# Kernel optimization log

Hardware: AMD Instinct MI355X
Metric: run time of the kernel (lower is better)

Reference implementation:

```python
import jax, jax.numpy as jnp
import numpy as np
from jax import lax

ITERATIONS = 8
GAMMA = 0.99
TEMPERATURE = 100.0
THRESHOLD_SCALE = 2.0
MIN_SOURCE = 1e-06


def maxpool3(x):
    # 3x3 max pool, stride 1, pad 1 (pad value -inf, matching torch MaxPool2d)
    return lax.reduce_window(x, -jnp.inf, lax.max, (1, 1, 3, 3), (1, 1, 1, 1),
                             [(0, 0), (0, 0), (1, 1), (1, 1)])


def _axis_coords(n_out, n_in, dtype):
    if n_out == 1:
        return jnp.zeros((1,), dtype=dtype)
    return jnp.arange(n_out, dtype=dtype) * ((n_in - 1) / (n_out - 1))


def resize_bilinear(x, out_h, out_w):
    # bilinear resize with align_corners=True, separable along H then W
    B, C, H, W = x.shape
    dt = x.dtype
    h = _axis_coords(out_h, H, dt)
    i0 = jnp.floor(h).astype(jnp.int32)
    i1 = jnp.minimum(i0 + 1, H - 1)
    wh = (h - i0.astype(dt))[None, None, :, None]
    x = x[:, :, i0, :] * (1 - wh) + x[:, :, i1, :] * wh
    w = _axis_coords(out_w, W, dt)
    j0 = jnp.floor(w).astype(jnp.int32)
    j1 = jnp.minimum(j0 + 1, W - 1)
    ww = (w - j0.astype(dt))[None, None, None, :]
    x = x[:, :, :, j0] * (1 - ww) + x[:, :, :, j1] * ww
    return x


def activation_mask(m):
    B, C, H, W = m.shape
    flat = m.reshape(B, C, H * W)
    mean = lax.stop_gradient(jnp.mean(flat, axis=-1))
    std = lax.stop_gradient(jnp.std(flat, axis=-1, ddof=1))  # torch std is unbiased
    thr = (mean + THRESHOLD_SCALE * std)[:, :, None, None]
    return jax.nn.sigmoid(TEMPERATURE * (m - thr)) + MIN_SOURCE


def propagate_field(init_field):
    B, C, H, W = init_field.shape
    cur = init_field
    down = maxpool3(init_field) * GAMMA  # level 0, stride 1
    cur = jnp.maximum(cur, down)
    stride = 1
    h, w = H, W
    for _ in range(1, ITERATIONS):
        stride *= 2
        h, w = h // 2, w // 2  # floor(size * 0.5)
        down = resize_bilinear(down, h, w)
        down = maxpool3(down) * (GAMMA ** stride)
        up = resize_bilinear(down, H, W)
        cur = jnp.maximum(cur, up)
    return cur


def setup_inputs() -> dict:
    key = jax.random.key(0)
    k1, k2, k3 = jax.random.split(key, 3)
    B, C, H, W = 4, 128, 256, 256
    Cm = C // 8
    x = jax.random.normal(k1, (B, C, H, W), dtype=jnp.float32)
    w1 = jax.random.normal(k2, (Cm, C), dtype=jnp.float32) * 0.05
    b1 = jnp.zeros((Cm,), dtype=jnp.float32)
    w2 = jax.random.normal(k3, (C, Cm), dtype=jnp.float32) * 0.05
    b2 = jnp.zeros((C,), dtype=jnp.float32)
    return {"x": x, "w1": w1, "b1": b1, "w2": w2, "b2": b2}


def reference(x, w1, b1, w2, b2):
    x_pos = jax.nn.relu(x)
    x_neg = jax.nn.relu(-x)
    L_pos = propagate_field(x_pos * activation_mask(x_pos))
    L_neg = propagate_field(x_neg * activation_mask(x_neg))
    radiance = L_pos - L_neg
    # receptor modulator: 1x1 conv -> relu -> 1x1 conv -> sigmoid
    h = jax.nn.relu(jnp.einsum('oc,bchw->bohw', w1, radiance) + b1[None, :, None, None])
    mod = jax.nn.sigmoid(jnp.einsum('oc,bchw->bohw', w2, h) + b2[None, :, None, None])
    return x * mod
```

## Files before the change

### kernel.cpp

```cpp
#include <hip/hip_runtime.h>
#include <cmath>

constexpr int BN = 4, CN = 128, HN = 256, WN = 256;
constexpr int NPLANE = BN * CN;
constexpr int PLANE  = HN * WN;

constexpr long long OF_THR = 0;
constexpr long long OF_R1  = 1024;
constexpr long long OF_D1  = OF_R1 + 2LL * NPLANE * 128 * 128;
constexpr long long OF_D2  = OF_D1 + 2LL * NPLANE * 128 * 128;
constexpr long long OF_D3  = OF_D2 + 2LL * NPLANE * 64 * 64;
constexpr long long OF_D4  = OF_D3 + 2LL * NPLANE * 32 * 32;
constexpr long long OF_D5  = OF_D4 + 2LL * NPLANE * 16 * 16;
constexpr long long OF_D6  = OF_D5 + 2LL * NPLANE * 8 * 8;
constexpr long long OF_D7  = OF_D6 + 2LL * NPLANE * 4 * 4;

static __device__ __forceinline__ float sigm100(float a, float thr) {
    return 1.f / (1.f + __expf(-100.f * (a - thr))) + 1e-6f;
}

__global__ __launch_bounds__(256) void statsA_kernel(const float* __restrict__ x,
                                                     float* __restrict__ ws) {
    const int strip = blockIdx.x;
    const int p = blockIdx.y;
    const int tid = threadIdx.x;
    const float* xp = x + (long long)p * PLANE + strip * 4096;
    float sp = 0, spp = 0, sn = 0, snn = 0;
    for (int i = tid; i < 4096; i += 256) {
        float v = xp[i];
        float a = fmaxf(v, 0.f), b = fmaxf(-v, 0.f);
        sp += a; spp += a * a;
        sn += b; snn += b * b;
    }
    __shared__ float red[256];
    float vals[4] = {sp, spp, sn, snn};
    float* dst = ws + OF_D1 + ((long long)p * 16 + strip) * 4;
    for (int q = 0; q < 4; q++) {
        red[tid] = vals[q];
        __syncthreads();
        for (int s = 128; s > 0; s >>= 1) {
            if (tid < s) red[tid] += red[tid + s];
            __syncthreads();
        }
        if (tid == 0) dst[q] = red[0];
        __syncthreads();
    }
}

__global__ __launch_bounds__(256) void statsB_kernel(float* __restrict__ ws) {
    int p = blockIdx.x * 256 + threadIdx.x;
    if (p >= 512) return;
    double sp = 0, spp = 0, sn = 0, snn = 0;
    for (int s = 0; s < 16; s++) {
        const float* src = ws + OF_D1 + ((long long)p * 16 + s) * 4;
        sp += src[0]; spp += src[1]; sn += src[2]; snn += src[3];
    }
    double N = (double)PLANE;
    double meanP = sp / N, meanN = sn / N;
    double varP = (spp - sp * sp / N) / (N - 1.0);
    double varN = (snn - sn * sn / N) / (N - 1.0);
    varP = varP > 0 ? varP : 0;
    varN = varN > 0 ? varN : 0;
    ws[OF_THR + p]       = (float)(meanP + 2.0 * sqrt(varP));
    ws[OF_THR + 512 + p] = (float)(meanN + 2.0 * sqrt(varN));
}

__global__ __launch_bounds__(256, 3) void field_kernel(const float* __restrict__ x,
                                                       float* __restrict__ ws) {
    const int tile = blockIdx.x;
    const int p = blockIdx.y;
    const int ty = tile >> 2, tx = tile & 3;
    const int y0 = ty * 64, x0 = tx * 64;
    const int tid = threadIdx.x;

    __shared__ float cf[66 * 66];
    __shared__ float plP[64 * 64];
    __shared__ float plN[64 * 64];

    const float thrP = ws[OF_THR + p];
    const float thrN = ws[OF_THR + 512 + p];
    const float* xp = x + (long long)p * PLANE;

    for (int i = tid; i < 66 * 66; i += 256) {
        int ly = i / 66, lx = i - ly * 66;
        int gy = min(max(y0 - 1 + ly, 0), 255);
        int gx = min(max(x0 - 1 + lx, 0), 255);
        float v = xp[gy * 256 + gx];
        float thr = v > 0.f ? thrP : thrN;
        cf[i] = v * sigm100(fabsf(v), thr);
    }
    __syncthreads();

    const float g1 = 0.99f;
    for (int i = tid; i < 64 * 64; i += 256) {
        int oy = i >> 6, ox = i & 63;
        const float* r0 = cf + oy * 66 + ox;
        const float* r1r = r0 + 66;
        const float* r2 = r1r + 66;
        float cmax = fmaxf(fmaxf(r0[0], r0[1]), r0[2]);
        float cmin = fminf(fminf(r0[0], r0[1]), r0[2]);
        cmax = fmaxf(cmax, fmaxf(fmaxf(r1r[0], r1r[1]), r1r[2]));
        cmin = fminf(cmin, fminf(fminf(r1r[0], r1r[1]), r1r[2]));
        cmax = fmaxf(cmax, fmaxf(fmaxf(r2[0], r2[1]), r2[2]));
        cmin = fminf(cmin, fminf(fminf(r2[0], r2[1]), r2[2]));
        plP[i] = fmaxf(cmax, 0.f) * g1;
        plN[i] = fmaxf(-cmin, 0.f) * g1;
    }
    __syncthreads();

    const float S = (float)(255.0 / 127.0);
    for (int i = tid; i < 32 * 32; i += 256) {
        int ry = i >> 5, rx = i & 31;
        int jy = ty * 32 + ry, jx = tx * 32 + rx;
        float uy = jy * S, ux = jx * S;
        int iy0 = (int)floorf(uy), ix0 = (int)floorf(ux);
        int iy1 = min(iy0 + 1, 255), ix1 = min(ix0 + 1, 255);
        float fy = uy - iy0, fx = ux - ix0;
        int ly0 = min(max(iy0 - y0, 0), 63), ly1 = min(max(iy1 - y0, 0), 63);
        int lx0 = min(max(ix0 - x0, 0), 63), lx1 = min(max(ix1 - x0, 0), 63);
        float aP = plP[ly0 * 64 + lx0], bP = plP[ly0 * 64 + lx1];
        float cP = plP[ly1 * 64 + lx0], dP = plP[ly1 * 64 + lx1];
        float vP = (aP * (1.f - fy) + cP * fy) * (1.f - fx) + (bP * (1.f - fy) + dP * fy) * fx;
        float aN = plN[ly0 * 64 + lx0], bN = plN[ly0 * 64 + lx1];
        float cN = plN[ly1 * 64 + lx0], dN = plN[ly1 * 64 + lx1];
        float vN = (aN * (1.f - fy) + cN * fy) * (1.f - fx) + (bN * (1.f - fy) + dN * fy) * fx;
        ws[OF_R1 + (long long)p * 16384 + jy * 128 + jx] = vP;
        ws[OF_R1 + (long long)(512 + p) * 16384 + jy * 128 + jx] = vN;
    }
}

__global__ __launch_bounds__(256) void pool1_kernel(float* __restrict__ ws, float gamma2) {
    long long gid = (long long)blockIdx.x * 256 + threadIdx.x;
    int ps = (int)(gid >> 14);
    int rem = (int)(gid & 16383);
    int oy = rem >> 7, ox = rem & 127;
    const float* src = ws + OF_R1 + (long long)ps * 16384;
    float m = -INFINITY;
    for (int dy = -1; dy <= 1; dy++) {
        int yy = oy + dy;
        if (yy < 0 || yy > 127) continue;
        for (int dx = -1; dx <= 1; dx++) {
            int xx = ox + dx;
            if (xx < 0 || xx > 127) continue;
            m = fmaxf(m, src[yy * 128 + xx]);
        }
    }
    ws[OF_D1 + (long long)ps * 16384 + rem] = m * gamma2;
}

__global__ __launch_bounds__(256) void pstep_kernel(float* __restrict__ ws,
                                                    long long srcOff, long long dstOff,
                                                    int m, int n, int logn,
                                                    float scale, float gamma) {
    int gid = blockIdx.x * 256 + threadIdx.x;
    int ps = gid >> (2 * logn);
    int rem = gid & ((1 << (2 * logn)) - 1);
    int oy = rem >> logn, ox = rem & ((1 << logn) - 1);
    const float* src = ws + srcOff + (long long)ps * m * m;
    float best = -INFINITY;
    for (int dy = -1; dy <= 1; dy++) {
        int yy = oy + dy;
        if (yy < 0 || yy >= n) continue;
        float uy = yy * scale;
        int iy0 = (int)floorf(uy);
        if (iy0 > m - 1) iy0 = m - 1;
        int iy1 = min(iy0 + 1, m - 1);
        float fy = uy - iy0;
        for (int dx = -1; dx <= 1; dx++) {
            int xx = ox + dx;
            if (xx < 0 || xx >= n) continue;
            float ux = xx * scale;
            int ix0 = (int)floorf(ux);
            if (ix0 > m - 1) ix0 = m - 1;
            int ix1 = min(ix0 + 1, m - 1);
            float fx = ux - ix0;
            float a = src[iy0 * m + ix0], b = src[iy0 * m + ix1];
            float c = src[iy1 * m + ix0], d = src[iy1 * m + ix1];
            float v = (a * (1.f - fy) + c * fy) * (1.f - fx) + (b * (1.f - fy) + d * fy) * fx;
            best = fmaxf(best, v);
        }
    }
    ws[dstOff + (long long)ps * n * n + rem] = best * gamma;
}

__global__ __launch_bounds__(256, 4) void radiance_kernel(const float* __restrict__ x,
                                                          const float* __restrict__ ws,
                                                          float* __restrict__ rad) {
    const int tY = blockIdx.x;
    const int p = blockIdx.y;
    const int Y0 = tY * 16;
    const int tid = threadIdx.x;

    __shared__ float cf[18 * 258];
    __shared__ float fpb[2 * 1920];

    const float thrP = ws[OF_THR + p];
    const float thrN = ws[OF_THR + 512 + p];
    const float* xp = x + (long long)p * PLANE;

    for (int r = 0; r < 18; r++) {
        int gy = min(max(Y0 - 1 + r, 0), 255);
        float v = xp[gy * 256 + tid];
        float thr = v > 0.f ? thrP : thrN;
        float c = v * sigm100(fabsf(v), thr);
        cf[r * 258 + tid + 1] = c;
        if (tid == 0) cf[r * 258] = c;
        if (tid == 255) cf[r * 258 + 257] = c;
    }

    int oyk[8], hyk[8], basek[8];
    int acc = 0;
#pragma unroll
    for (int k = 1; k <= 7; k++) {
        int n = 256 >> k;
        float sc = (float)(n - 1) / 255.f;
        int oy = (int)floorf(Y0 * sc);
        int ey = (int)floorf((Y0 + 15) * sc) + 1;
        if (ey > n - 1) ey = n - 1;
        oyk[k] = oy; hyk[k] = ey - oy + 1; basek[k] = acc;
        acc += hyk[k] * n;
    }
    const long long OFD[8] = {0, OF_D1, OF_D2, OF_D3, OF_D4, OF_D5, OF_D6, OF_D7};
    for (int s = 0; s < 2; s++) {
#pragma unroll
        for (int k = 1; k <= 7; k++) {
            int n = 256 >> k;
            const float* src = ws + OFD[k] + (long long)(s * 512 + p) * n * n + oyk[k] * n;
            float* dst = fpb + s * 1920 + basek[k];
            int tot = hyk[k] * n;
            for (int i = tid; i < tot; i += 256) dst[i] = src[i];
        }
    }
    __syncthreads();

    int j0[8], j1[8]; float fxk[8];
#pragma unroll
    for (int k = 1; k <= 7; k++) {
        int n = 256 >> k;
        float sc = (float)(n - 1) / 255.f;
        float ux = tid * sc;
        int a = (int)ux; if (a > n - 1) a = n - 1;
        j0[k] = a; j1[k] = min(a + 1, n - 1);
        fxk[k] = ux - (float)a;
    }

    float xl0P[8], xl1P[8], xl0N[8], xl1N[8];
    int cy[8];
#pragma unroll
    for (int k = 1; k <= 7; k++) {
        int n = 256 >> k;
        int i0 = oyk[k];
        int i1 = min(i0 + 1, n - 1);
        cy[k] = i0;
        int r1o = (i1 - oyk[k]) * n;
        float aP = fpb[basek[k] + j0[k]],        bP = fpb[basek[k] + j1[k]];
        float cP = fpb[basek[k] + r1o + j0[k]],  dP = fpb[basek[k] + r1o + j1[k]];
        xl0P[k] = aP + fxk[k] * (bP - aP);
        xl1P[k] = cP + fxk[k] * (dP - cP);
        float aN = fpb[1920 + basek[k] + j0[k]],       bN = fpb[1920 + basek[k] + j1[k]];
        float cN = fpb[1920 + basek[k] + r1o + j0[k]], dN = fpb[1920 + basek[k] + r1o + j1[k]];
        xl0N[k] = aN + fxk[k] * (bN - aN);
        xl1N[k] = cN + fxk[k] * (dN - cN);
    }

    float hx0, hx1, hx2, hn0, hn1, hn2, cc1, cc2;
    {
        int b0 = 0 * 258 + tid;
        float a = cf[b0], b = cf[b0 + 1], c = cf[b0 + 2];
        hx0 = fmaxf(fmaxf(a, b), c); hn0 = fminf(fminf(a, b), c);
        int b1 = 1 * 258 + tid;
        float d = cf[b1], e = cf[b1 + 1], f = cf[b1 + 2];
        hx1 = fmaxf(fmaxf(d, e), f); hn1 = fminf(fminf(d, e), f);
        cc1 = e;
    }

    float* radp = rad + (long long)p * PLANE + (long long)Y0 * 256 + tid;

    for (int q = 0; q < 16; q++) {
        int bn = (q + 2) * 258 + tid;
        float a = cf[bn], b = cf[bn + 1], c = cf[bn + 2];
        hx2 = fmaxf(fmaxf(a, b), c); hn2 = fminf(fminf(a, b), c);
        cc2 = b;

        float poolmax = fmaxf(fmaxf(hx0, hx1), hx2);
        float poolmin = fminf(fminf(hn0, hn1), hn2);
        float mP = fmaxf(fmaxf(cc1, 0.f), 0.99f * fmaxf(poolmax, 0.f));
        float mN = fmaxf(fmaxf(-cc1, 0.f), 0.99f * fmaxf(-poolmin, 0.f));

        int row = Y0 + q;
#pragma unroll
        for (int k = 1; k <= 7; k++) {
            int n = 256 >> k;
            float sc = (float)(n - 1) / 255.f;
            float uy = row * sc;
            int i0 = (int)uy;
            if (i0 != cy[k]) {
                cy[k] = i0;
                xl0P[k] = xl1P[k]; xl0N[k] = xl1N[k];
                int i1 = min(i0 + 1, n - 1);
                int ro = (i1 - oyk[k]) * n;
                float aP = fpb[basek[k] + ro + j0[k]], bP = fpb[basek[k] + ro + j1[k]];
                xl1P[k] = aP + fxk[k] * (bP - aP);
                float aN = fpb[1920 + basek[k] + ro + j0[k]], bN = fpb[1920 + basek[k] + ro + j1[k]];
                xl1N[k] = aN + fxk[k] * (bN - aN);
            }
            float fy = uy - (float)i0;
            mP = fmaxf(mP, xl0P[k] + fy * (xl1P[k] - xl0P[k]));
            mN = fmaxf(mN, xl0N[k] + fy * (xl1N[k] - xl0N[k]));
        }
        radp[q * 256] = mP - mN;

        hx0 = hx1; hx1 = hx2;
        hn0 = hn1; hn1 = hn2;
        cc1 = cc2;
    }
}

__global__ __launch_bounds__(256) void mlp_kernel(const float* __restrict__ x,
                                                  const float* __restrict__ w1,
                                                  const float* __restrict__ b1,
                                                  const float* __restrict__ w2,
                                                  const float* __restrict__ b2,
                                                  float* io) {
    const int y = blockIdx.x;
    const int b = blockIdx.y;
    const int col = threadIdx.x;

    float h[16];
#pragma unroll
    for (int o = 0; o < 16; o++) h[o] = b1[o];
    for (int c = 0; c < 128; c++) {
        float r = io[(long long)(b * 128 + c) * PLANE + y * 256 + col];
#pragma unroll
        for (int o = 0; o < 16; o++) h[o] += w1[o * 128 + c] * r;
    }
#pragma unroll
    for (int o = 0; o < 16; o++) h[o] = fmaxf(h[o], 0.f);
    for (int c = 0; c < 128; c++) {
        float z = b2[c];
#pragma unroll
        for (int o = 0; o < 16; o++) z += w2[c * 16 + o] * h[o];
        float mod = 1.f / (1.f + __expf(-z));
        long long idx = (long long)(b * 128 + c) * PLANE + y * 256 + col;
        io[idx] = x[idx] * mod;
    }
}

extern "C" void kernel_launch(void* const* d_in, const int* in_sizes, int n_in,
                              void* d_out, int out_size, void* d_ws, size_t ws_size,
                              hipStream_t stream) {
    (void)in_sizes; (void)n_in; (void)out_size; (void)ws_size;
    const float* x  = (const float*)d_in[0];
    const float* w1 = (const float*)d_in[1];
    const float* b1 = (const float*)d_in[2];
    const float* w2 = (const float*)d_in[3];
    const float* b2 = (const float*)d_in[4];
    float* out = (float*)d_out;
    float* ws = (float*)d_ws;

    statsA_kernel<<<dim3(16, 512), 256, 0, stream>>>(x, ws);
    statsB_kernel<<<2, 256, 0, stream>>>(ws);
    field_kernel<<<dim3(16, 512), 256, 0, stream>>>(x, ws);
    pool1_kernel<<<(1024 * 16384) / 256, 256, 0, stream>>>(ws, (float)std::pow(0.99, 2.0));

    const long long dsts[8] = {0, OF_D1, OF_D2, OF_D3, OF_D4, OF_D5, OF_D6, OF_D7};
    for (int k = 2; k <= 7; k++) {
        int m = 256 >> (k - 1), n = 256 >> k;
        int logn = 8 - k;
        float scale = (float)((double)(m - 1) / (double)(n - 1));
        float gamma = (float)std::pow(0.99, (double)(1 << k));
        int total = 1024 * n * n;
        pstep_kernel<<<total / 256, 256, 0, stream>>>(ws, dsts[k - 1], dsts[k],
                                                      m, n, logn, scale, gamma);
    }
    radiance_kernel<<<dim3(16, 512), 256, 0, stream>>>(x, ws, out);
    mlp_kernel<<<dim3(256, 4), 256, 0, stream>>>(x, w1, b1, w2, b2, out);
}
```

Baseline: 880.2 us.

## Fuse pyramid levels into one LDS-resident kernel and stream level-1 rows in radiance

Replaces the pool1 launch and the six pstep launches with a single pyramid_kernel. It builds each plane's whole downsample pyramid in shared memory and writes every level to global memory. field_kernel now computes the 3x3 pool directly at the four bilinear taps instead of staging full pooled tiles in LDS, which frees shared memory and raises the occupancy hint. radiance_kernel no longer stages the large level-1 slab; it double-buffers two 128-wide rows from global memory as needed, adding barriers inside the row loop. The intent is to remove launch overhead and global round trips between pyramid levels and to raise occupancy, at the cost of 1024 fairly heavy single-plane blocks with large LDS use.

```diff
diff --git a/kernel.cpp b/kernel.cpp
--- a/kernel.cpp
+++ b/kernel.cpp
@@ -65,7 +65,19 @@
     ws[OF_THR + 512 + p] = (float)(meanN + 2.0 * sqrt(varN));
 }
 
-__global__ __launch_bounds__(256, 3) void field_kernel(const float* __restrict__ x,
+#define POOL9(LY, LX, MX, MN)                                                 \
+    {   const float* q_ = cf + (LY) * 66 + (LX);                              \
+        float t0 = q_[0],   t1 = q_[1],   t2 = q_[2];                         \
+        float u0 = q_[66],  u1 = q_[67],  u2 = q_[68];                        \
+        float w0 = q_[132], w1 = q_[133], w2 = q_[134];                       \
+        MX = fmaxf(fmaxf(fmaxf(t0, t1), t2),                                  \
+             fmaxf(fmaxf(fmaxf(u0, u1), u2),                                  \
+                   fmaxf(fmaxf(w0, w1), w2)));                                \
+        MN = fminf(fminf(fminf(t0, t1), t2),                                  \
+             fminf(fminf(fminf(u0, u1), u2),                                  \
+                   fminf(fminf(w0, w1), w2))); }
+
+__global__ __launch_bounds__(256, 8) void field_kernel(const float* __restrict__ x,
                                                        float* __restrict__ ws) {
     const int tile = blockIdx.x;
     const int p = blockIdx.y;
@@ -74,8 +86,6 @@
     const int tid = threadIdx.x;
 
     __shared__ float cf[66 * 66];
-    __shared__ float plP[64 * 64];
-    __shared__ float plN[64 * 64];
 
     const float thrP = ws[OF_THR + p];
     const float thrN = ws[OF_THR + 512 + p];
@@ -92,22 +102,6 @@
     __syncthreads();
 
     const float g1 = 0.99f;
-    for (int i = tid; i < 64 * 64; i += 256) {
-        int oy = i >> 6, ox = i & 63;
-        const float* r0 = cf + oy * 66 + ox;
-        const float* r1r = r0 + 66;
-        const float* r2 = r1r + 66;
-        float cmax = fmaxf(fmaxf(r0[0], r0[1]), r0[2]);
-        float cmin = fminf(fminf(r0[0], r0[1]), r0[2]);
-        cmax = fmaxf(cmax, fmaxf(fmaxf(r1r[0], r1r[1]), r1r[2]));
-        cmin = fminf(cmin, fminf(fminf(r1r[0], r1r[1]), r1r[2]));
-        cmax = fmaxf(cmax, fmaxf(fmaxf(r2[0], r2[1]), r2[2]));
-        cmin = fminf(cmin, fminf(fminf(r2[0], r2[1]), r2[2]));
-        plP[i] = fmaxf(cmax, 0.f) * g1;
-        plN[i] = fmaxf(-cmin, 0.f) * g1;
-    }
-    __syncthreads();
-
     const float S = (float)(255.0 / 127.0);
     for (int i = tid; i < 32 * 32; i += 256) {
         int ry = i >> 5, rx = i & 31;
@@ -118,72 +112,98 @@
         float fy = uy - iy0, fx = ux - ix0;
         int ly0 = min(max(iy0 - y0, 0), 63), ly1 = min(max(iy1 - y0, 0), 63);
         int lx0 = min(max(ix0 - x0, 0), 63), lx1 = min(max(ix1 - x0, 0), 63);
-        float aP = plP[ly0 * 64 + lx0], bP = plP[ly0 * 64 + lx1];
-        float cP = plP[ly1 * 64 + lx0], dP = plP[ly1 * 64 + lx1];
+
+        float amx, amn, bmx, bmn, cmx, cmn, dmx, dmn;
+        POOL9(ly0, lx0, amx, amn)
+        POOL9(ly0, lx1, bmx, bmn)
+        POOL9(ly1, lx0, cmx, cmn)
+        POOL9(ly1, lx1, dmx, dmn)
+
+        float aP = fmaxf(amx, 0.f) * g1, bP = fmaxf(bmx, 0.f) * g1;
+        float cP = fmaxf(cmx, 0.f) * g1, dP = fmaxf(dmx, 0.f) * g1;
         float vP = (aP * (1.f - fy) + cP * fy) * (1.f - fx) + (bP * (1.f - fy) + dP * fy) * fx;
-        float aN = plN[ly0 * 64 + lx0], bN = plN[ly0 * 64 + lx1];
-        float cN = plN[ly1 * 64 + lx0], dN = plN[ly1 * 64 + lx1];
+        float aN = fmaxf(-amn, 0.f) * g1, bN = fmaxf(-bmn, 0.f) * g1;
+        float cN = fmaxf(-cmn, 0.f) * g1, dN = fmaxf(-dmn, 0.f) * g1;
         float vN = (aN * (1.f - fy) + cN * fy) * (1.f - fx) + (bN * (1.f - fy) + dN * fy) * fx;
         ws[OF_R1 + (long long)p * 16384 + jy * 128 + jx] = vP;
         ws[OF_R1 + (long long)(512 + p) * 16384 + jy * 128 + jx] = vN;
     }
 }
 
-__global__ __launch_bounds__(256) void pool1_kernel(float* __restrict__ ws, float gamma2) {
-    long long gid = (long long)blockIdx.x * 256 + threadIdx.x;
-    int ps = (int)(gid >> 14);
-    int rem = (int)(gid & 16383);
-    int oy = rem >> 7, ox = rem & 127;
+__global__ __launch_bounds__(256, 2) void pyramid_kernel(float* __restrict__ ws) {
+    const int ps = blockIdx.x;
+    const int tid = threadIdx.x;
+    __shared__ float A[16384];
+    __shared__ float B[4096];
+
     const float* src = ws + OF_R1 + (long long)ps * 16384;
-    float m = -INFINITY;
-    for (int dy = -1; dy <= 1; dy++) {
-        int yy = oy + dy;
-        if (yy < 0 || yy > 127) continue;
-        for (int dx = -1; dx <= 1; dx++) {
-            int xx = ox + dx;
-            if (xx < 0 || xx > 127) continue;
-            m = fmaxf(m, src[yy * 128 + xx]);
-        }
-    }
-    ws[OF_D1 + (long long)ps * 16384 + rem] = m * gamma2;
-}
-
-__global__ __launch_bounds__(256) void pstep_kernel(float* __restrict__ ws,
-                                                    long long srcOff, long long dstOff,
-                                                    int m, int n, int logn,
-                                                    float scale, float gamma) {
-    int gid = blockIdx.x * 256 + threadIdx.x;
-    int ps = gid >> (2 * logn);
-    int rem = gid & ((1 << (2 * logn)) - 1);
-    int oy = rem >> logn, ox = rem & ((1 << logn) - 1);
-    const float* src = ws + srcOff + (long long)ps * m * m;
-    float best = -INFINITY;
-    for (int dy = -1; dy <= 1; dy++) {
-        int yy = oy + dy;
-        if (yy < 0 || yy >= n) continue;
-        float uy = yy * scale;
-        int iy0 = (int)floorf(uy);
-        if (iy0 > m - 1) iy0 = m - 1;
-        int iy1 = min(iy0 + 1, m - 1);
-        float fy = uy - iy0;
-        for (int dx = -1; dx <= 1; dx++) {
-            int xx = ox + dx;
-            if (xx < 0 || xx >= n) continue;
-            float ux = xx * scale;
-            int ix0 = (int)floorf(ux);
-            if (ix0 > m - 1) ix0 = m - 1;
-            int ix1 = min(ix0 + 1, m - 1);
-            float fx = ux - ix0;
-            float a = src[iy0 * m + ix0], b = src[iy0 * m + ix1];
-            float c = src[iy1 * m + ix0], d = src[iy1 * m + ix1];
-            float v = (a * (1.f - fy) + c * fy) * (1.f - fx) + (b * (1.f - fy) + d * fy) * fx;
-            best = fmaxf(best, v);
-        }
-    }
-    ws[dstOff + (long long)ps * n * n + rem] = best * gamma;
-}
-
-__global__ __launch_bounds__(256, 4) void radiance_kernel(const float* __restrict__ x,
+    float* d1 = ws + OF_D1 + (long long)ps * 16384;
+    double gd = 0.99 * 0.99;
+    {
+        float g2 = (float)gd;
+        for (int i = tid; i < 16384; i += 256) {
+            int oy = i >> 7, ox = i & 127;
+            float m = -INFINITY;
+            for (int dy = -1; dy <= 1; dy++) {
+                int yy = oy + dy;
+                if (yy < 0 || yy > 127) continue;
+                for (int dx = -1; dx <= 1; dx++) {
+                    int xx = ox + dx;
+                    if (xx < 0 || xx > 127) continue;
+                    m = fmaxf(m, src[yy * 128 + xx]);
+                }
+            }
+            float v = m * g2;
+            d1[i] = v; A[i] = v;
+        }
+    }
+    __syncthreads();
+
+    const long long OFD[8] = {0, OF_D1, OF_D2, OF_D3, OF_D4, OF_D5, OF_D6, OF_D7};
+    float* curL = A;
+    float* nxtL = B;
+#pragma unroll
+    for (int k = 2; k <= 7; k++) {
+        const int m = 256 >> (k - 1), n = 256 >> k;
+        const int logn = 8 - k;
+        gd = gd * gd;
+        const float gamma = (float)gd;
+        const float scale = (float)((double)(m - 1) / (double)(n - 1));
+        float* dst = ws + OFD[k] + (long long)ps * n * n;
+        for (int i = tid; i < n * n; i += 256) {
+            int oy = i >> logn, ox = i & (n - 1);
+            float best = -INFINITY;
+            for (int dy = -1; dy <= 1; dy++) {
+                int yy = oy + dy;
+                if (yy < 0 || yy >= n) continue;
+                float uy = yy * scale;
+                int iy0 = (int)floorf(uy);
+                if (iy0 > m - 1) iy0 = m - 1;
+                int iy1 = min(iy0 + 1, m - 1);
+                float fy = uy - iy0;
+                for (int dx = -1; dx <= 1; dx++) {
+                    int xx = ox + dx;
+                    if (xx < 0 || xx >= n) continue;
+                    float ux = xx * scale;
+                    int ix0 = (int)floorf(ux);
+                    if (ix0 > m - 1) ix0 = m - 1;
+                    int ix1 = min(ix0 + 1, m - 1);
+                    float fx = ux - ix0;
+                    float a = curL[iy0 * m + ix0], b = curL[iy0 * m + ix1];
+                    float c = curL[iy1 * m + ix0], d = curL[iy1 * m + ix1];
+                    float v = (a * (1.f - fy) + c * fy) * (1.f - fx) + (b * (1.f - fy) + d * fy) * fx;
+                    best = fmaxf(best, v);
+                }
+            }
+            float o = best * gamma;
+            dst[i] = o; nxtL[i] = o;
+        }
+        __syncthreads();
+        float* t = curL; curL = nxtL; nxtL = t;
+    }
+}
+
+__global__ __launch_bounds__(256, 6) void radiance_kernel(const float* __restrict__ x,
                                                           const float* __restrict__ ws,
                                                           float* __restrict__ rad) {
     const int tY = blockIdx.x;
@@ -192,7 +212,9 @@
     const int tid = threadIdx.x;
 
     __shared__ float cf[18 * 258];
-    __shared__ float fpb[2 * 1920];
+    __shared__ float fpb[2 * 600];
+    __shared__ float fp1P[2 * 128];
+    __shared__ float fp1N[2 * 128];
 
     const float thrP = ws[OF_THR + p];
     const float thrN = ws[OF_THR + 512 + p];
@@ -208,10 +230,11 @@
         if (tid == 255) cf[r * 258 + 257] = c;
     }
 
+    const long long OFD[8] = {0, OF_D1, OF_D2, OF_D3, OF_D4, OF_D5, OF_D6, OF_D7};
     int oyk[8], hyk[8], basek[8];
     int acc = 0;
 #pragma unroll
-    for (int k = 1; k <= 7; k++) {
+    for (int k = 2; k <= 7; k++) {
         int n = 256 >> k;
         float sc = (float)(n - 1) / 255.f;
         int oy = (int)floorf(Y0 * sc);
@@ -220,22 +243,37 @@
         oyk[k] = oy; hyk[k] = ey - oy + 1; basek[k] = acc;
         acc += hyk[k] * n;
     }
-    const long long OFD[8] = {0, OF_D1, OF_D2, OF_D3, OF_D4, OF_D5, OF_D6, OF_D7};
     for (int s = 0; s < 2; s++) {
 #pragma unroll
-        for (int k = 1; k <= 7; k++) {
+        for (int k = 2; k <= 7; k++) {
             int n = 256 >> k;
-            const float* src = ws + OFD[k] + (long long)(s * 512 + p) * n * n + oyk[k] * n;
-            float* dst = fpb + s * 1920 + basek[k];
+            const float* srcp = ws + OFD[k] + (long long)(s * 512 + p) * n * n + oyk[k] * n;
+            float* dstp = fpb + s * 600 + basek[k];
             int tot = hyk[k] * n;
-            for (int i = tid; i < tot; i += 256) dst[i] = src[i];
+            for (int i = tid; i < tot; i += 256) dstp[i] = srcp[i];
+        }
+    }
+
+    const float sc1 = 127.f / 255.f;
+    const float* gP1 = ws + OF_D1 + (long long)p * 16384;
+    const float* gN1 = gP1 + 512LL * 16384;
+    int cy1 = (int)floorf(Y0 * sc1);
+    {
+        int i1 = min(cy1 + 1, 127);
+        int c = tid & 127;
+        if (tid < 128) {
+            fp1P[0 * 128 + c] = gP1[cy1 * 128 + c];
+            fp1P[1 * 128 + c] = gP1[i1 * 128 + c];
+        } else {
+            fp1N[0 * 128 + c] = gN1[cy1 * 128 + c];
+            fp1N[1 * 128 + c] = gN1[i1 * 128 + c];
         }
     }
     __syncthreads();
 
     int j0[8], j1[8]; float fxk[8];
 #pragma unroll
-    for (int k = 1; k <= 7; k++) {
+    for (int k = 2; k <= 7; k++) {
         int n = 256 >> k;
         float sc = (float)(n - 1) / 255.f;
         float ux = tid * sc;
@@ -243,11 +281,18 @@
         j0[k] = a; j1[k] = min(a + 1, n - 1);
         fxk[k] = ux - (float)a;
     }
+    int j0_1, j1_1; float fx1;
+    {
+        float ux = tid * sc1;
+        int a = (int)ux; if (a > 127) a = 127;
+        j0_1 = a; j1_1 = min(a + 1, 127);
+        fx1 = ux - (float)a;
+    }
 
     float xl0P[8], xl1P[8], xl0N[8], xl1N[8];
     int cy[8];
 #pragma unroll
-    for (int k = 1; k <= 7; k++) {
+    for (int k = 2; k <= 7; k++) {
         int n = 256 >> k;
         int i0 = oyk[k];
         int i1 = min(i0 + 1, n - 1);
@@ -257,10 +302,22 @@
         float cP = fpb[basek[k] + r1o + j0[k]],  dP = fpb[basek[k] + r1o + j1[k]];
         xl0P[k] = aP + fxk[k] * (bP - aP);
         xl1P[k] = cP + fxk[k] * (dP - cP);
-        float aN = fpb[1920 + basek[k] + j0[k]],       bN = fpb[1920 + basek[k] + j1[k]];
-        float cN = fpb[1920 + basek[k] + r1o + j0[k]], dN = fpb[1920 + basek[k] + r1o + j1[k]];
+        float aN = fpb[600 + basek[k] + j0[k]],       bN = fpb[600 + basek[k] + j1[k]];
+        float cN = fpb[600 + basek[k] + r1o + j0[k]], dN = fpb[600 + basek[k] + r1o + j1[k]];
         xl0N[k] = aN + fxk[k] * (bN - aN);
         xl1N[k] = cN + fxk[k] * (dN - cN);
+    }
+    float xl0P1, xl1P1, xl0N1, xl1N1;
+    int cur1 = 1;
+    {
+        float a = fp1P[0 * 128 + j0_1], e = fp1P[0 * 128 + j1_1];
+        float c = fp1P[1 * 128 + j0_1], d = fp1P[1 * 128 + j1_1];
+        xl0P1 = a + fx1 * (e - a);
+        xl1P1 = c + fx1 * (d - c);
+        float an = fp1N[0 * 128 + j0_1], en = fp1N[0 * 128 + j1_1];
+        float cn = fp1N[1 * 128 + j0_1], dn = fp1N[1 * 128 + j1_1];
+        xl0N1 = an + fx1 * (en - an);
+        xl1N1 = cn + fx1 * (dn - cn);
     }
 
     float hx0, hx1, hx2, hn0, hn1, hn2, cc1, cc2;
@@ -288,8 +345,33 @@
         float mN = fmaxf(fmaxf(-cc1, 0.f), 0.99f * fmaxf(-poolmin, 0.f));
 
         int row = Y0 + q;
-#pragma unroll
-        for (int k = 1; k <= 7; k++) {
+
+        {
+            float uy = row * sc1;
+            int i0 = (int)uy;
+            if (i0 != cy1) {
+                cy1 = i0;
+                xl0P1 = xl1P1; xl0N1 = xl1N1;
+                int i1n = min(i0 + 1, 127);
+                int slot = cur1 ^ 1;
+                __syncthreads();
+                int cc = tid & 127;
+                if (tid < 128) fp1P[slot * 128 + cc] = gP1[i1n * 128 + cc];
+                else           fp1N[slot * 128 + cc] = gN1[i1n * 128 + cc];
+                __syncthreads();
+                float aa = fp1P[slot * 128 + j0_1], ee = fp1P[slot * 128 + j1_1];
+                xl1P1 = aa + fx1 * (ee - aa);
+                float an = fp1N[slot * 128 + j0_1], en = fp1N[slot * 128 + j1_1];
+                xl1N1 = an + fx1 * (en - an);
+                cur1 = slot;
+            }
+            float fy = uy - (float)i0;
+            mP = fmaxf(mP, xl0P1 + fy * (xl1P1 - xl0P1));
+            mN = fmaxf(mN, xl0N1 + fy * (xl1N1 - xl0N1));
+        }
+
+#pragma unroll
+        for (int k = 2; k <= 7; k++) {
             int n = 256 >> k;
             float sc = (float)(n - 1) / 255.f;
             float uy = row * sc;
@@ -301,7 +383,7 @@
                 int ro = (i1 - oyk[k]) * n;
                 float aP = fpb[basek[k] + ro + j0[k]], bP = fpb[basek[k] + ro + j1[k]];
                 xl1P[k] = aP + fxk[k] * (bP - aP);
-                float aN = fpb[1920 + basek[k] + ro + j0[k]], bN = fpb[1920 + basek[k] + ro + j1[k]];
+                float aN = fpb[600 + basek[k] + ro + j0[k]], bN = fpb[600 + basek[k] + ro + j1[k]];
                 xl1N[k] = aN + fxk[k] * (bN - aN);
             }
             float fy = uy - (float)i0;
@@ -361,18 +443,7 @@
     statsA_kernel<<<dim3(16, 512), 256, 0, stream>>>(x, ws);
     statsB_kernel<<<2, 256, 0, stream>>>(ws);
     field_kernel<<<dim3(16, 512), 256, 0, stream>>>(x, ws);
-    pool1_kernel<<<(1024 * 16384) / 256, 256, 0, stream>>>(ws, (float)std::pow(0.99, 2.0));
-
-    const long long dsts[8] = {0, OF_D1, OF_D2, OF_D3, OF_D4, OF_D5, OF_D6, OF_D7};
-    for (int k = 2; k <= 7; k++) {
-        int m = 256 >> (k - 1), n = 256 >> k;
-        int logn = 8 - k;
-        float scale = (float)((double)(m - 1) / (double)(n - 1));
-        float gamma = (float)std::pow(0.99, (double)(1 << k));
-        int total = 1024 * n * n;
-        pstep_kernel<<<total / 256, 256, 0, stream>>>(ws, dsts[k - 1], dsts[k],
-                                                      m, n, logn, scale, gamma);
-    }
+    pyramid_kernel<<<1024, 256, 0, stream>>>(ws);
     radiance_kernel<<<dim3(16, 512), 256, 0, stream>>>(x, ws, out);
     mlp_kernel<<<dim3(256, 4), 256, 0, stream>>>(x, w1, b1, w2, b2, out);
 }
```

Result: slower. 944.0 us (+7.2%).

## Fuse pyramid levels into one kernel, recompute pool in field, halve radiance row tile

Applied to the files above, without the earlier changes.

The six per-level pyramid launches become a single kernel with one block per plane. Level 2 is read from global memory and the smaller levels are ping-ponged through shared memory, which removes launch overhead and global round trips between levels. field_kernel no longer stages the pooled plane in shared memory. It recomputes the 3x3 max/min at the four bilinear taps it needs, which lowers LDS use and raises the occupancy bound to 8. radiance_kernel now processes 8 rows per block instead of 16 and launches twice as many blocks, trading more redundant halo and pyramid staging for more parallelism.

```diff
diff --git a/kernel.cpp b/kernel.cpp
--- a/kernel.cpp
+++ b/kernel.cpp
@@ -65,7 +65,19 @@
     ws[OF_THR + 512 + p] = (float)(meanN + 2.0 * sqrt(varN));
 }
 
-__global__ __launch_bounds__(256, 3) void field_kernel(const float* __restrict__ x,
+#define POOL9(LY, LX, MX, MN)                                                 \
+    {   const float* q_ = cf + (LY) * 66 + (LX);                              \
+        float t0 = q_[0],   t1 = q_[1],   t2 = q_[2];                         \
+        float u0 = q_[66],  u1 = q_[67],  u2 = q_[68];                        \
+        float w0 = q_[132], w1 = q_[133], w2 = q_[134];                       \
+        MX = fmaxf(fmaxf(fmaxf(t0, t1), t2),                                  \
+             fmaxf(fmaxf(fmaxf(u0, u1), u2),                                  \
+                   fmaxf(fmaxf(w0, w1), w2)));                                \
+        MN = fminf(fminf(fminf(t0, t1), t2),                                  \
+             fminf(fminf(fminf(u0, u1), u2),                                  \
+                   fminf(fminf(w0, w1), w2))); }
+
+__global__ __launch_bounds__(256, 8) void field_kernel(const float* __restrict__ x,
                                                        float* __restrict__ ws) {
     const int tile = blockIdx.x;
     const int p = blockIdx.y;
@@ -74,8 +86,6 @@
     const int tid = threadIdx.x;
 
     __shared__ float cf[66 * 66];
-    __shared__ float plP[64 * 64];
-    __shared__ float plN[64 * 64];
 
     const float thrP = ws[OF_THR + p];
     const float thrN = ws[OF_THR + 512 + p];
@@ -92,22 +102,6 @@
     __syncthreads();
 
     const float g1 = 0.99f;
-    for (int i = tid; i < 64 * 64; i += 256) {
-        int oy = i >> 6, ox = i & 63;
-        const float* r0 = cf + oy * 66 + ox;
-        const float* r1r = r0 + 66;
-        const float* r2 = r1r + 66;
-        float cmax = fmaxf(fmaxf(r0[0], r0[1]), r0[2]);
-        float cmin = fminf(fminf(r0[0], r0[1]), r0[2]);
-        cmax = fmaxf(cmax, fmaxf(fmaxf(r1r[0], r1r[1]), r1r[2]));
-        cmin = fminf(cmin, fminf(fminf(r1r[0], r1r[1]), r1r[2]));
-        cmax = fmaxf(cmax, fmaxf(fmaxf(r2[0], r2[1]), r2[2]));
-        cmin = fminf(cmin, fminf(fminf(r2[0], r2[1]), r2[2]));
-        plP[i] = fmaxf(cmax, 0.f) * g1;
-        plN[i] = fmaxf(-cmin, 0.f) * g1;
-    }
-    __syncthreads();
-
     const float S = (float)(255.0 / 127.0);
     for (int i = tid; i < 32 * 32; i += 256) {
         int ry = i >> 5, rx = i & 31;
@@ -118,11 +112,18 @@
         float fy = uy - iy0, fx = ux - ix0;
         int ly0 = min(max(iy0 - y0, 0), 63), ly1 = min(max(iy1 - y0, 0), 63);
         int lx0 = min(max(ix0 - x0, 0), 63), lx1 = min(max(ix1 - x0, 0), 63);
-        float aP = plP[ly0 * 64 + lx0], bP = plP[ly0 * 64 + lx1];
-        float cP = plP[ly1 * 64 + lx0], dP = plP[ly1 * 64 + lx1];
+
+        float amx, amn, bmx, bmn, cmx, cmn, dmx, dmn;
+        POOL9(ly0, lx0, amx, amn)
+        POOL9(ly0, lx1, bmx, bmn)
+        POOL9(ly1, lx0, cmx, cmn)
+        POOL9(ly1, lx1, dmx, dmn)
+
+        float aP = fmaxf(amx, 0.f) * g1, bP = fmaxf(bmx, 0.f) * g1;
+        float cP = fmaxf(cmx, 0.f) * g1, dP = fmaxf(dmx, 0.f) * g1;
         float vP = (aP * (1.f - fy) + cP * fy) * (1.f - fx) + (bP * (1.f - fy) + dP * fy) * fx;
-        float aN = plN[ly0 * 64 + lx0], bN = plN[ly0 * 64 + lx1];
-        float cN = plN[ly1 * 64 + lx0], dN = plN[ly1 * 64 + lx1];
+        float aN = fmaxf(-amn, 0.f) * g1, bN = fmaxf(-bmn, 0.f) * g1;
+        float cN = fmaxf(-cmn, 0.f) * g1, dN = fmaxf(-dmn, 0.f) * g1;
         float vN = (aN * (1.f - fy) + cN * fy) * (1.f - fx) + (bN * (1.f - fy) + dN * fy) * fx;
         ws[OF_R1 + (long long)p * 16384 + jy * 128 + jx] = vP;
         ws[OF_R1 + (long long)(512 + p) * 16384 + jy * 128 + jx] = vN;
@@ -148,57 +149,115 @@
     ws[OF_D1 + (long long)ps * 16384 + rem] = m * gamma2;
 }
 
-__global__ __launch_bounds__(256) void pstep_kernel(float* __restrict__ ws,
-                                                    long long srcOff, long long dstOff,
-                                                    int m, int n, int logn,
-                                                    float scale, float gamma) {
-    int gid = blockIdx.x * 256 + threadIdx.x;
-    int ps = gid >> (2 * logn);
-    int rem = gid & ((1 << (2 * logn)) - 1);
-    int oy = rem >> logn, ox = rem & ((1 << logn) - 1);
-    const float* src = ws + srcOff + (long long)ps * m * m;
-    float best = -INFINITY;
-    for (int dy = -1; dy <= 1; dy++) {
-        int yy = oy + dy;
-        if (yy < 0 || yy >= n) continue;
-        float uy = yy * scale;
-        int iy0 = (int)floorf(uy);
-        if (iy0 > m - 1) iy0 = m - 1;
-        int iy1 = min(iy0 + 1, m - 1);
-        float fy = uy - iy0;
-        for (int dx = -1; dx <= 1; dx++) {
-            int xx = ox + dx;
-            if (xx < 0 || xx >= n) continue;
-            float ux = xx * scale;
-            int ix0 = (int)floorf(ux);
-            if (ix0 > m - 1) ix0 = m - 1;
-            int ix1 = min(ix0 + 1, m - 1);
-            float fx = ux - ix0;
-            float a = src[iy0 * m + ix0], b = src[iy0 * m + ix1];
-            float c = src[iy1 * m + ix0], d = src[iy1 * m + ix1];
-            float v = (a * (1.f - fy) + c * fy) * (1.f - fx) + (b * (1.f - fy) + d * fy) * fx;
-            best = fmaxf(best, v);
-        }
-    }
-    ws[dstOff + (long long)ps * n * n + rem] = best * gamma;
-}
+__global__ __launch_bounds__(256) void pyramid_rest_kernel(float* __restrict__ ws) {
+    const int ps = blockIdx.x;
+    const int tid = threadIdx.x;
+    __shared__ float A[4096];
+    __shared__ float B[1024];
+
+    const long long OFD[8] = {0, OF_D1, OF_D2, OF_D3, OF_D4, OF_D5, OF_D6, OF_D7};
+    double gd = 0.99 * 0.99;
+
+    {
+        const int m = 128, n = 64, logn = 6;
+        gd = gd * gd;
+        const float gamma = (float)gd;
+        const float scale = (float)(127.0 / 63.0);
+        const float* src = ws + OF_D1 + (long long)ps * 16384;
+        float* dst = ws + OF_D2 + (long long)ps * n * n;
+        for (int i = tid; i < n * n; i += 256) {
+            int oy = i >> logn, ox = i & (n - 1);
+            float best = -INFINITY;
+            for (int dy = -1; dy <= 1; dy++) {
+                int yy = oy + dy;
+                if (yy < 0 || yy >= n) continue;
+                float uy = yy * scale;
+                int iy0 = (int)floorf(uy);
+                if (iy0 > m - 1) iy0 = m - 1;
+                int iy1 = min(iy0 + 1, m - 1);
+                float fy = uy - iy0;
+                for (int dx = -1; dx <= 1; dx++) {
+                    int xx = ox + dx;
+                    if (xx < 0 || xx >= n) continue;
+                    float ux = xx * scale;
+                    int ix0 = (int)floorf(ux);
+                    if (ix0 > m - 1) ix0 = m - 1;
+                    int ix1 = min(ix0 + 1, m - 1);
+                    float fx = ux - ix0;
+                    float a = src[iy0 * m + ix0], b = src[iy0 * m + ix1];
+                    float c = src[iy1 * m + ix0], d = src[iy1 * m + ix1];
+                    float v = (a * (1.f - fy) + c * fy) * (1.f - fx) + (b * (1.f - fy) + d * fy) * fx;
+                    best = fmaxf(best, v);
+                }
+            }
+            float o = best * gamma;
+            dst[i] = o; A[i] = o;
+        }
+    }
+    __syncthreads();
+
+    float* curL = A;
+    float* nxtL = B;
+#pragma unroll
+    for (int k = 3; k <= 7; k++) {
+        const int m = 256 >> (k - 1), n = 256 >> k;
+        const int logn = 8 - k;
+        gd = gd * gd;
+        const float gamma = (float)gd;
+        const float scale = (float)((double)(m - 1) / (double)(n - 1));
+        float* dst = ws + OFD[k] + (long long)ps * n * n;
+        for (int i = tid; i < n * n; i += 256) {
+            int oy = i >> logn, ox = i & (n - 1);
+            float best = -INFINITY;
+            for (int dy = -1; dy <= 1; dy++) {
+                int yy = oy + dy;
+                if (yy < 0 || yy >= n) continue;
+                float uy = yy * scale;
+                int iy0 = (int)floorf(uy);
+                if (iy0 > m - 1) iy0 = m - 1;
+                int iy1 = min(iy0 + 1, m - 1);
+                float fy = uy - iy0;
+                for (int dx = -1; dx <= 1; dx++) {
+                    int xx = ox + dx;
+                    if (xx < 0 || xx >= n) continue;
+                    float ux = xx * scale;
+                    int ix0 = (int)floorf(ux);
+                    if (ix0 > m - 1) ix0 = m - 1;
+                    int ix1 = min(ix0 + 1, m - 1);
+                    float fx = ux - ix0;
+                    float a = curL[iy0 * m + ix0], b = curL[iy0 * m + ix1];
+                    float c = curL[iy1 * m + ix0], d = curL[iy1 * m + ix1];
+                    float v = (a * (1.f - fy) + c * fy) * (1.f - fx) + (b * (1.f - fy) + d * fy) * fx;
+                    best = fmaxf(best, v);
+                }
+            }
+            float o = best * gamma;
+            dst[i] = o; nxtL[i] = o;
+        }
+        __syncthreads();
+        float* t = curL; curL = nxtL; nxtL = t;
+    }
+}
+
+constexpr int QBLK = 8;
+constexpr int FPW  = 1216;
 
 __global__ __launch_bounds__(256, 4) void radiance_kernel(const float* __restrict__ x,
                                                           const float* __restrict__ ws,
                                                           float* __restrict__ rad) {
     const int tY = blockIdx.x;
     const int p = blockIdx.y;
-    const int Y0 = tY * 16;
+    const int Y0 = tY * QBLK;
     const int tid = threadIdx.x;
 
-    __shared__ float cf[18 * 258];
-    __shared__ float fpb[2 * 1920];
+    __shared__ float cf[(QBLK + 2) * 258];
+    __shared__ float fpb[2 * FPW];
 
     const float thrP = ws[OF_THR + p];
     const float thrN = ws[OF_THR + 512 + p];
     const float* xp = x + (long long)p * PLANE;
 
-    for (int r = 0; r < 18; r++) {
+    for (int r = 0; r < QBLK + 2; r++) {
         int gy = min(max(Y0 - 1 + r, 0), 255);
         float v = xp[gy * 256 + tid];
         float thr = v > 0.f ? thrP : thrN;
@@ -215,7 +274,7 @@
         int n = 256 >> k;
         float sc = (float)(n - 1) / 255.f;
         int oy = (int)floorf(Y0 * sc);
-        int ey = (int)floorf((Y0 + 15) * sc) + 1;
+        int ey = (int)floorf((Y0 + QBLK - 1) * sc) + 1;
         if (ey > n - 1) ey = n - 1;
         oyk[k] = oy; hyk[k] = ey - oy + 1; basek[k] = acc;
         acc += hyk[k] * n;
@@ -226,7 +285,7 @@
         for (int k = 1; k <= 7; k++) {
             int n = 256 >> k;
             const float* src = ws + OFD[k] + (long long)(s * 512 + p) * n * n + oyk[k] * n;
-            float* dst = fpb + s * 1920 + basek[k];
+            float* dst = fpb + s * FPW + basek[k];
             int tot = hyk[k] * n;
             for (int i = tid; i < tot; i += 256) dst[i] = src[i];
         }
@@ -257,8 +316,8 @@
         float cP = fpb[basek[k] + r1o + j0[k]],  dP = fpb[basek[k] + r1o + j1[k]];
         xl0P[k] = aP + fxk[k] * (bP - aP);
         xl1P[k] = cP + fxk[k] * (dP - cP);
-        float aN = fpb[1920 + basek[k] + j0[k]],       bN = fpb[1920 + basek[k] + j1[k]];
-        float cN = fpb[1920 + basek[k] + r1o + j0[k]], dN = fpb[1920 + basek[k] + r1o + j1[k]];
+        float aN = fpb[FPW + basek[k] + j0[k]],       bN = fpb[FPW + basek[k] + j1[k]];
+        float cN = fpb[FPW + basek[k] + r1o + j0[k]], dN = fpb[FPW + basek[k] + r1o + j1[k]];
         xl0N[k] = aN + fxk[k] * (bN - aN);
         xl1N[k] = cN + fxk[k] * (dN - cN);
     }
@@ -276,7 +335,7 @@
 
     float* radp = rad + (long long)p * PLANE + (long long)Y0 * 256 + tid;
 
-    for (int q = 0; q < 16; q++) {
+    for (int q = 0; q < QBLK; q++) {
         int bn = (q + 2) * 258 + tid;
         float a = cf[bn], b = cf[bn + 1], c = cf[bn + 2];
         hx2 = fmaxf(fmaxf(a, b), c); hn2 = fminf(fminf(a, b), c);
@@ -301,7 +360,7 @@
                 int ro = (i1 - oyk[k]) * n;
                 float aP = fpb[basek[k] + ro + j0[k]], bP = fpb[basek[k] + ro + j1[k]];
                 xl1P[k] = aP + fxk[k] * (bP - aP);
-                float aN = fpb[1920 + basek[k] + ro + j0[k]], bN = fpb[1920 + basek[k] + ro + j1[k]];
+                float aN = fpb[FPW + basek[k] + ro + j0[k]], bN = fpb[FPW + basek[k] + ro + j1[k]];
                 xl1N[k] = aN + fxk[k] * (bN - aN);
             }
             float fy = uy - (float)i0;
@@ -362,17 +421,7 @@
     statsB_kernel<<<2, 256, 0, stream>>>(ws);
     field_kernel<<<dim3(16, 512), 256, 0, stream>>>(x, ws);
     pool1_kernel<<<(1024 * 16384) / 256, 256, 0, stream>>>(ws, (float)std::pow(0.99, 2.0));
-
-    const long long dsts[8] = {0, OF_D1, OF_D2, OF_D3, OF_D4, OF_D5, OF_D6, OF_D7};
-    for (int k = 2; k <= 7; k++) {
-        int m = 256 >> (k - 1), n = 256 >> k;
-        int logn = 8 - k;
-        float scale = (float)((double)(m - 1) / (double)(n - 1));
-        float gamma = (float)std::pow(0.99, (double)(1 << k));
-        int total = 1024 * n * n;
-        pstep_kernel<<<total / 256, 256, 0, stream>>>(ws, dsts[k - 1], dsts[k],
-                                                      m, n, logn, scale, gamma);
-    }
-    radiance_kernel<<<dim3(16, 512), 256, 0, stream>>>(x, ws, out);
+    pyramid_rest_kernel<<<1024, 256, 0, stream>>>(ws);
+    radiance_kernel<<<dim3(32, 512), 256, 0, stream>>>(x, ws, out);
     mlp_kernel<<<dim3(256, 4), 256, 0, stream>>>(x, w1, b1, w2, b2, out);
 }
```

Result: slower. 910.9 us (+3.5%).
